# Optimization experiments

Measured on AMD Instinct MI355X. Metric: run time of the kernel, lower is better.

Reference implementation:

```python
import jax, jax.numpy as jnp
import numpy as np

# Polynomial coefficients from the original module (hard-coded in forward).
P00, P10, P20, P30 = 0.0, 0.0, 0.0, 0.0      # identity-kernel branch (all zero)
P01, P11, P21 = -0.000287, 0.266, -0.1097    # learned-weight branch
STRIDE, PAD = 1, 1


def _conv(x, w):
    # NCHW input, OIHW kernel -> NCHW output. Equivalent to
    # unfold(x).T @ w.view(O,-1).T reshaped back, i.e. torch's im2col matmul.
    return jax.lax.conv_general_dilated(
        x, w,
        window_strides=(STRIDE, STRIDE),
        padding=[(PAD, PAD), (PAD, PAD)],
        dimension_numbers=('NCHW', 'OIHW', 'NCHW'))


def setup_inputs() -> dict:
    key = jax.random.key(0)
    k1, k2 = jax.random.split(key)
    img = jax.random.normal(k1, (16, 64, 128, 128), dtype=jnp.float32)
    # weights initialized N(0, 0.8) in the original module
    weights = jax.random.normal(k2, (64, 64, 3, 3), dtype=jnp.float32) * 0.8
    identity_kernel = jnp.ones((64, 64, 3, 3), dtype=jnp.float32)
    return {"img": img, "weights": weights, "identity_kernel": identity_kernel}


def reference(img, weights, identity_kernel):
    kh, kw = weights.shape[2], weights.shape[3]
    # Elementwise polynomial applied to the input, then contracted against
    # the (identity, learned) kernels. matmul-with-unfold == convolution,
    # so we express it as two convs instead of materializing im2col.
    poly_id = P00 + P10 * img + P20 * img**2 + P30 * img**3  # == zeros here
    poly_w = P01 + P11 * img + P21 * img**2
    out = _conv(poly_id, identity_kernel) + _conv(poly_w, weights)
    return out / (3 * kh * kw)
```

## Files before the change

### kernel.cpp

```cpp
#include <hip/hip_runtime.h>


typedef __bf16 bf16;
typedef __attribute__((ext_vector_type(8))) __bf16 bf16x8;
typedef __attribute__((ext_vector_type(16))) float f32x16;

static constexpr float A0 = -0.000287f / 27.0f;
static constexpr float A1 =  0.266f    / 27.0f;
static constexpr float A2 = -0.1097f   / 27.0f;

#define NN 16
#define CI 64
#define HH 128
#define WW 128
#define OO 64
#define LDS_BYTES 74112

__global__ void repack_w(const float* __restrict__ w, bf16* __restrict__ wrb) {
    int idx = blockIdx.x * 256 + threadIdx.x;
    if (idx >= 9 * 8 * 64 * 8) return;
    int cj    = idx & 7;
    int o     = (idx >> 3) & 63;
    int cc8   = (idx >> 9) & 7;
    int slice = idx >> 12;
    int ky = slice / 3, kx = slice - ky * 3;
    int c = cc8 * 8 + cj;
    wrb[idx] = (bf16)w[((o * CI + c) * 3 + ky) * 3 + kx];
}

__global__ __launch_bounds__(512, 4) void conv_mfma(const float* __restrict__ img,
                                                    const bf16* __restrict__ wrb,
                                                    float* __restrict__ out) {
    extern __shared__ __align__(16) char smem[];
    float* raw  = (float*)smem;
    bf16*  ilds = (bf16*)(smem + 49152);

    const int tid = threadIdx.x;
    const int b   = blockIdx.x;
    const int y0  = (b & 31) * 4;
    const int n   = b >> 5;

    const int wv   = tid >> 6;
    const int lane = tid & 63;
    const int lm   = lane & 31;
    const int half = lane >> 5;
    const int yl   = wv >> 1;
    const int Xh   = (wv & 1) * 64;

    auto dma = [&](int chunk) {
        const int ch = 2 * wv + half;
        const int x0 = (lane & 31) * 4;
        #pragma unroll
        for (int i = 0; i < 6; ++i) {
            const int yi = y0 - 1 + i;
            if ((unsigned)yi < 128u) {
                const float* g = img + ((n * CI + chunk * 16 + ch) * HH + yi) * WW + x0;
                __builtin_amdgcn_global_load_lds(
                    (const __attribute__((address_space(1))) void*)g,
                    (__attribute__((address_space(3))) void*)(raw + (wv + 8 * i) * 256),
                    16, 0, 0);
            }
        }
    };

    auto transform = [&]() {
        for (int t = tid; t < 780; t += 512) {
            int r   = t / 130;
            int rem = t - r * 130;
            int ccl = rem / 65;
            int xh  = rem - ccl * 65;
            int yi  = y0 - 1 + r;
            bf16* rowp = ilds + (r * 2 + ccl) * (130 * 8);
            if (xh < 64) {
                bf16x8 pk0, pk1;
                if ((unsigned)yi < 128u) {
                    const float* p = raw + (r * 16 + ccl * 8) * 128 + 2 * xh;
                    #pragma unroll
                    for (int j = 0; j < 8; ++j) {
                        float2 v = *(const float2*)(p + j * 128);
                        pk0[j] = (bf16)(A0 + v.x * (A1 + A2 * v.x));
                        pk1[j] = (bf16)(A0 + v.y * (A1 + A2 * v.y));
                    }
                } else {
                    #pragma unroll
                    for (int j = 0; j < 8; ++j) { pk0[j] = (bf16)0.0f; pk1[j] = (bf16)0.0f; }
                }
                *(bf16x8*)(rowp + (2 * xh + 1) * 8) = pk0;
                *(bf16x8*)(rowp + (2 * xh + 2) * 8) = pk1;
            } else {
                bf16x8 z;
                #pragma unroll
                for (int j = 0; j < 8; ++j) z[j] = (bf16)0.0f;
                *(bf16x8*)(rowp + 0) = z;
                *(bf16x8*)(rowp + 129 * 8) = z;
            }
        }
    };

    f32x16 acc[2][2];
    #pragma unroll
    for (int i = 0; i < 2; ++i)
        #pragma unroll
        for (int j = 0; j < 2; ++j)
            #pragma unroll
            for (int k = 0; k < 16; ++k) acc[i][j][k] = 0.0f;

    const bf16x8* wfr = (const bf16x8*)wrb;
    const bf16x8* ifr = (const bf16x8*)ilds;

    const int corder = ((b >> 8) & 1) * 2;

    dma(corder);
    __syncthreads();

    for (int j = 0; j < 4; ++j) {
        const int cc = (corder + j) & 3;
        transform();
        __syncthreads();
        if (j < 3) dma((corder + j + 1) & 3);
        const int cc8g = cc * 2 + half;
        #pragma unroll
        for (int ky = 0; ky < 3; ++ky) {
            const int r = yl + ky;
            #pragma unroll
            for (int kx = 0; kx < 3; ++kx) {
                const int slice = ky * 3 + kx;
                bf16x8 a0 = wfr[(slice * 8 + cc8g) * 64 + lm];
                bf16x8 a1 = wfr[(slice * 8 + cc8g) * 64 + 32 + lm];
                const int ib = (r * 2 + half) * 130 + Xh + lm + kx;
                bf16x8 b0 = ifr[ib];
                bf16x8 b1 = ifr[ib + 32];
                acc[0][0] = __builtin_amdgcn_mfma_f32_32x32x16_bf16(a0, b0, acc[0][0], 0, 0, 0);
                acc[0][1] = __builtin_amdgcn_mfma_f32_32x32x16_bf16(a0, b1, acc[0][1], 0, 0, 0);
                acc[1][0] = __builtin_amdgcn_mfma_f32_32x32x16_bf16(a1, b0, acc[1][0], 0, 0, 0);
                acc[1][1] = __builtin_amdgcn_mfma_f32_32x32x16_bf16(a1, b1, acc[1][1], 0, 0, 0);
            }
        }
        if (j < 3) __syncthreads();
    }

    const int ybase = (n * OO * HH + (y0 + yl)) * WW;
    #pragma unroll
    for (int p = 0; p < 2; ++p)
        #pragma unroll
        for (int xt = 0; xt < 2; ++xt) {
            const int x = Xh + xt * 32 + lm;
            #pragma unroll
            for (int rg = 0; rg < 16; ++rg) {
                const int o = (rg & 3) + 8 * (rg >> 2) + 4 * half + 32 * p;
                out[ybase + o * (HH * WW) + x] = acc[p][xt][rg];
            }
        }
}

extern "C" void kernel_launch(void* const* d_in, const int* in_sizes, int n_in,
                              void* d_out, int out_size, void* d_ws, size_t ws_size,
                              hipStream_t stream) {
    const float* img = (const float*)d_in[0];
    const float* w   = (const float*)d_in[1];
    float* out = (float*)d_out;
    bf16* wrb  = (bf16*)d_ws;

    static bool attr_done = false;
    if (!attr_done) {
        (void)hipFuncSetAttribute((const void*)conv_mfma,
                                  hipFuncAttributeMaxDynamicSharedMemorySize, LDS_BYTES);
        attr_done = true;
    }

    repack_w<<<(9 * 8 * 64 * 8 + 255) / 256, 256, 0, stream>>>(w, wrb);
    conv_mfma<<<NN * (HH / 4), 512, LDS_BYTES, stream>>>(img, wrb, out);
}
```

Before: 128.3 us.

## Double-buffer 8-channel raw slices to overlap DMA with transform and MFMA

Splits each 16-channel chunk into two 8-channel halves held in two raw LDS slots, so the global-to-LDS load of the next half is issued while the current half is transformed and the MFMAs run. The aim is to hide global load latency that the old one-chunk-at-a-time schedule exposed. In exchange there are more barriers per chunk (8 half-steps instead of 4 steps), only 390 of 512 threads do the transform, and the per-block channel-order stagger is dropped.

```diff
diff --git a/kernel.cpp b/kernel.cpp
--- a/kernel.cpp
+++ b/kernel.cpp
@@ -32,8 +32,8 @@
                                                     const bf16* __restrict__ wrb,
                                                     float* __restrict__ out) {
     extern __shared__ __align__(16) char smem[];
-    float* raw  = (float*)smem;
-    bf16*  ilds = (bf16*)(smem + 49152);
+    float* slots = (float*)smem;
+    bf16*  ilds  = (bf16*)(smem + 49152);
 
     const int tid = threadIdx.x;
     const int b   = blockIdx.x;
@@ -47,34 +47,36 @@
     const int yl   = wv >> 1;
     const int Xh   = (wv & 1) * 64;
 
-    auto dma = [&](int chunk) {
-        const int ch = 2 * wv + half;
-        const int x0 = (lane & 31) * 4;
-        #pragma unroll
-        for (int i = 0; i < 6; ++i) {
-            const int yi = y0 - 1 + i;
+    auto dma = [&](int h, int i0, int i1) {
+        float* slot = slots + (h & 1) * 6144;
+        const int cb = h * 8;
+        for (int i = i0; i < i1; ++i) {
+            const int q   = wv + 8 * i;
+            const int r   = q >> 2;
+            const int ch0 = (2 * q) & 7;
+            const int yi  = y0 - 1 + r;
             if ((unsigned)yi < 128u) {
-                const float* g = img + ((n * CI + chunk * 16 + ch) * HH + yi) * WW + x0;
+                const float* g = img + ((n * CI + cb + ch0 + half) * HH + yi) * WW + lm * 4;
                 __builtin_amdgcn_global_load_lds(
                     (const __attribute__((address_space(1))) void*)g,
-                    (__attribute__((address_space(3))) void*)(raw + (wv + 8 * i) * 256),
+                    (__attribute__((address_space(3))) void*)(slot + q * 256),
                     16, 0, 0);
             }
         }
     };
 
-    auto transform = [&]() {
-        for (int t = tid; t < 780; t += 512) {
-            int r   = t / 130;
-            int rem = t - r * 130;
-            int ccl = rem / 65;
-            int xh  = rem - ccl * 65;
-            int yi  = y0 - 1 + r;
+    auto transform = [&](int h) {
+        const float* slot = slots + (h & 1) * 6144;
+        const int ccl = h & 1;
+        if (tid < 390) {
+            const int r  = tid / 65;
+            const int xh = tid - r * 65;
+            const int yi = y0 - 1 + r;
             bf16* rowp = ilds + (r * 2 + ccl) * (130 * 8);
             if (xh < 64) {
                 bf16x8 pk0, pk1;
                 if ((unsigned)yi < 128u) {
-                    const float* p = raw + (r * 16 + ccl * 8) * 128 + 2 * xh;
+                    const float* p = slot + (r * 8) * 128 + 2 * xh;
                     #pragma unroll
                     for (int j = 0; j < 8; ++j) {
                         float2 v = *(const float2*)(p + j * 128);
@@ -108,35 +110,36 @@
     const bf16x8* wfr = (const bf16x8*)wrb;
     const bf16x8* ifr = (const bf16x8*)ilds;
 
-    const int corder = ((b >> 8) & 1) * 2;
+    dma(0, 0, 3);
 
-    dma(corder);
-    __syncthreads();
-
-    for (int j = 0; j < 4; ++j) {
-        const int cc = (corder + j) & 3;
-        transform();
+    for (int h = 0; h < 8; ++h) {
         __syncthreads();
-        if (j < 3) dma((corder + j + 1) & 3);
-        const int cc8g = cc * 2 + half;
-        #pragma unroll
-        for (int ky = 0; ky < 3; ++ky) {
-            const int r = yl + ky;
+        if (h < 7) dma(h + 1, 0, 2);
+        transform(h);
+        if (h & 1) {
+            __syncthreads();
+            if (h < 7) dma(h + 1, 2, 3);
+            const int cc8g = (h >> 1) * 2 + half;
             #pragma unroll
-            for (int kx = 0; kx < 3; ++kx) {
-                const int slice = ky * 3 + kx;
-                bf16x8 a0 = wfr[(slice * 8 + cc8g) * 64 + lm];
-                bf16x8 a1 = wfr[(slice * 8 + cc8g) * 64 + 32 + lm];
-                const int ib = (r * 2 + half) * 130 + Xh + lm + kx;
-                bf16x8 b0 = ifr[ib];
-                bf16x8 b1 = ifr[ib + 32];
-                acc[0][0] = __builtin_amdgcn_mfma_f32_32x32x16_bf16(a0, b0, acc[0][0], 0, 0, 0);
-                acc[0][1] = __builtin_amdgcn_mfma_f32_32x32x16_bf16(a0, b1, acc[0][1], 0, 0, 0);
-                acc[1][0] = __builtin_amdgcn_mfma_f32_32x32x16_bf16(a1, b0, acc[1][0], 0, 0, 0);
-                acc[1][1] = __builtin_amdgcn_mfma_f32_32x32x16_bf16(a1, b1, acc[1][1], 0, 0, 0);
+            for (int ky = 0; ky < 3; ++ky) {
+                const int r = yl + ky;
+                #pragma unroll
+                for (int kx = 0; kx < 3; ++kx) {
+                    const int slice = ky * 3 + kx;
+                    bf16x8 a0 = wfr[(slice * 8 + cc8g) * 64 + lm];
+                    bf16x8 a1 = wfr[(slice * 8 + cc8g) * 64 + 32 + lm];
+                    const int ib = (r * 2 + half) * 130 + Xh + lm + kx;
+                    bf16x8 b0 = ifr[ib];
+                    bf16x8 b1 = ifr[ib + 32];
+                    acc[0][0] = __builtin_amdgcn_mfma_f32_32x32x16_bf16(a0, b0, acc[0][0], 0, 0, 0);
+                    acc[0][1] = __builtin_amdgcn_mfma_f32_32x32x16_bf16(a0, b1, acc[0][1], 0, 0, 0);
+                    acc[1][0] = __builtin_amdgcn_mfma_f32_32x32x16_bf16(a1, b0, acc[1][0], 0, 0, 0);
+                    acc[1][1] = __builtin_amdgcn_mfma_f32_32x32x16_bf16(a1, b1, acc[1][1], 0, 0, 0);
+                }
             }
+        } else {
+            if (h < 7) dma(h + 1, 2, 3);
         }
-        if (j < 3) __syncthreads();
     }
 
     const int ybase = (n * OO * HH + (y0 + yl)) * WW;
```

Result: slower. 134.1 us (+4.5%).

## Register-staged double-buffered input pipeline with smaller blocks and swizzled block order

Applied to the files above, without the earlier changes.

Replaces the global_load_lds raw staging plus a separate transform pass with direct global loads into registers. The polynomial is applied in registers and the bf16 result is written into a double-buffered LDS tile, so the next channel chunk loads while MFMAs run on the current one. Blocks shrink to 256 threads covering 2 output rows, which cuts LDS use and allows more resident blocks. Block indices are also remapped, which changes how blocks spread across XCDs. In exchange, each block recomputes more halo rows (4 input rows per 2 output rows) and register pressure rises.

```diff
diff --git a/kernel.cpp b/kernel.cpp
--- a/kernel.cpp
+++ b/kernel.cpp
@@ -14,11 +14,10 @@
 #define HH 128
 #define WW 128
 #define OO 64
-#define LDS_BYTES 74112
 
 __global__ void repack_w(const float* __restrict__ w, bf16* __restrict__ wrb) {
     int idx = blockIdx.x * 256 + threadIdx.x;
-    if (idx >= 9 * 8 * 64 * 8) return;
+    if (idx >= 36864) return;
     int cj    = idx & 7;
     int o     = (idx >> 3) & 63;
     int cc8   = (idx >> 9) & 7;
@@ -28,17 +27,16 @@
     wrb[idx] = (bf16)w[((o * CI + c) * 3 + ky) * 3 + kx];
 }
 
-__global__ __launch_bounds__(512, 4) void conv_mfma(const float* __restrict__ img,
+__global__ __launch_bounds__(256, 4) void conv_mfma(const float* __restrict__ img,
                                                     const bf16* __restrict__ wrb,
                                                     float* __restrict__ out) {
-    extern __shared__ __align__(16) char smem[];
-    float* raw  = (float*)smem;
-    bf16*  ilds = (bf16*)(smem + 49152);
+    __shared__ __align__(16) bf16 ilds[2][8320];
 
-    const int tid = threadIdx.x;
-    const int b   = blockIdx.x;
-    const int y0  = (b & 31) * 4;
-    const int n   = b >> 5;
+    const int tid  = threadIdx.x;
+    const int braw = blockIdx.x;
+    const int b    = (braw & 7) * 128 + (braw >> 3);
+    const int y0   = (b & 63) * 2;
+    const int n    = b >> 6;
 
     const int wv   = tid >> 6;
     const int lane = tid & 63;
@@ -47,53 +45,41 @@
     const int yl   = wv >> 1;
     const int Xh   = (wv & 1) * 64;
 
-    auto dma = [&](int chunk) {
-        const int ch = 2 * wv + half;
-        const int x0 = (lane & 31) * 4;
-        #pragma unroll
-        for (int i = 0; i < 6; ++i) {
-            const int yi = y0 - 1 + i;
-            if ((unsigned)yi < 128u) {
-                const float* g = img + ((n * CI + chunk * 16 + ch) * HH + yi) * WW + x0;
-                __builtin_amdgcn_global_load_lds(
-                    (const __attribute__((address_space(1))) void*)g,
-                    (__attribute__((address_space(3))) void*)(raw + (wv + 8 * i) * 256),
-                    16, 0, 0);
-            }
+    auto stage_load = [&](int chunk, int it, float2* v) {
+        const int id = tid + (it << 8);
+        const int r = id >> 7, ccl = (id >> 6) & 1, xh = id & 63;
+        const int yi = y0 - 1 + r;
+        if ((unsigned)yi < 128u) {
+            const float* p = img + ((n * CI + chunk * 16 + ccl * 8) * HH + yi) * WW + 2 * xh;
+            #pragma unroll
+            for (int j = 0; j < 8; ++j) v[j] = *(const float2*)(p + j * HH * WW);
         }
     };
-
-    auto transform = [&]() {
-        for (int t = tid; t < 780; t += 512) {
-            int r   = t / 130;
-            int rem = t - r * 130;
-            int ccl = rem / 65;
-            int xh  = rem - ccl * 65;
-            int yi  = y0 - 1 + r;
-            bf16* rowp = ilds + (r * 2 + ccl) * (130 * 8);
-            if (xh < 64) {
-                bf16x8 pk0, pk1;
-                if ((unsigned)yi < 128u) {
-                    const float* p = raw + (r * 16 + ccl * 8) * 128 + 2 * xh;
-                    #pragma unroll
-                    for (int j = 0; j < 8; ++j) {
-                        float2 v = *(const float2*)(p + j * 128);
-                        pk0[j] = (bf16)(A0 + v.x * (A1 + A2 * v.x));
-                        pk1[j] = (bf16)(A0 + v.y * (A1 + A2 * v.y));
-                    }
-                } else {
-                    #pragma unroll
-                    for (int j = 0; j < 8; ++j) { pk0[j] = (bf16)0.0f; pk1[j] = (bf16)0.0f; }
-                }
-                *(bf16x8*)(rowp + (2 * xh + 1) * 8) = pk0;
-                *(bf16x8*)(rowp + (2 * xh + 2) * 8) = pk1;
-            } else {
-                bf16x8 z;
-                #pragma unroll
-                for (int j = 0; j < 8; ++j) z[j] = (bf16)0.0f;
-                *(bf16x8*)(rowp + 0) = z;
-                *(bf16x8*)(rowp + 129 * 8) = z;
+    auto stage_write = [&](int buf, int it, float2* v) {
+        const int id = tid + (it << 8);
+        const int r = id >> 7, ccl = (id >> 6) & 1, xh = id & 63;
+        const int yi = y0 - 1 + r;
+        bf16* rowp = &ilds[buf][(r * 2 + ccl) * (130 * 8)];
+        bf16x8 pk0, pk1;
+        if ((unsigned)yi < 128u) {
+            #pragma unroll
+            for (int j = 0; j < 8; ++j) {
+                pk0[j] = (bf16)(A0 + v[j].x * (A1 + A2 * v[j].x));
+                pk1[j] = (bf16)(A0 + v[j].y * (A1 + A2 * v[j].y));
             }
+        } else {
+            #pragma unroll
+            for (int j = 0; j < 8; ++j) { pk0[j] = (bf16)0.0f; pk1[j] = (bf16)0.0f; }
+        }
+        *(bf16x8*)(rowp + (2 * xh + 1) * 8) = pk0;
+        *(bf16x8*)(rowp + (2 * xh + 2) * 8) = pk1;
+        if (it == 0 && tid < 8) {
+            bf16* hp = &ilds[buf][((tid >> 1) * 2 + (tid & 1)) * (130 * 8)];
+            bf16x8 z;
+            #pragma unroll
+            for (int j = 0; j < 8; ++j) z[j] = (bf16)0.0f;
+            *(bf16x8*)(hp + 0) = z;
+            *(bf16x8*)(hp + 129 * 8) = z;
         }
     };
 
@@ -106,19 +92,19 @@
             for (int k = 0; k < 16; ++k) acc[i][j][k] = 0.0f;
 
     const bf16x8* wfr = (const bf16x8*)wrb;
-    const bf16x8* ifr = (const bf16x8*)ilds;
 
-    const int corder = ((b >> 8) & 1) * 2;
+    {
+        float2 v[8];
+        stage_load(0, 0, v); stage_write(0, 0, v);
+        stage_load(0, 1, v); stage_write(0, 1, v);
+    }
 
-    dma(corder);
-    __syncthreads();
-
-    for (int j = 0; j < 4; ++j) {
-        const int cc = (corder + j) & 3;
-        transform();
+    for (int chunk = 0; chunk < 4; ++chunk) {
         __syncthreads();
-        if (j < 3) dma((corder + j + 1) & 3);
-        const int cc8g = cc * 2 + half;
+        float2 v[8];
+        if (chunk < 3) stage_load(chunk + 1, 0, v);
+        const bf16x8* ifr = (const bf16x8*)ilds[chunk & 1];
+        const int cc8g = chunk * 2 + half;
         #pragma unroll
         for (int ky = 0; ky < 3; ++ky) {
             const int r = yl + ky;
@@ -136,7 +122,12 @@
                 acc[1][1] = __builtin_amdgcn_mfma_f32_32x32x16_bf16(a1, b1, acc[1][1], 0, 0, 0);
             }
         }
-        if (j < 3) __syncthreads();
+        if (chunk < 3) {
+            const int nb = (chunk + 1) & 1;
+            stage_write(nb, 0, v);
+            stage_load(chunk + 1, 1, v);
+            stage_write(nb, 1, v);
+        }
     }
 
     const int ybase = (n * OO * HH + (y0 + yl)) * WW;
@@ -161,13 +152,6 @@
     float* out = (float*)d_out;
     bf16* wrb  = (bf16*)d_ws;
 
-    static bool attr_done = false;
-    if (!attr_done) {
-        (void)hipFuncSetAttribute((const void*)conv_mfma,
-                                  hipFuncAttributeMaxDynamicSharedMemorySize, LDS_BYTES);
-        attr_done = true;
-    }
-
-    repack_w<<<(9 * 8 * 64 * 8 + 255) / 256, 256, 0, stream>>>(w, wrb);
-    conv_mfma<<<NN * (HH / 4), 512, LDS_BYTES, stream>>>(img, wrb, out);
+    repack_w<<<(36864 + 255) / 256, 256, 0, stream>>>(w, wrb);
+    conv_mfma<<<NN * (HH / 2), 256, 0, stream>>>(img, wrb, out);
 }
```

Result: no change. 130.6 us (+1.8%).
